# Performance work log

Hardware: AMD Instinct MI355X
Metric: run time of the kernel (lower is better)

The kernel has to match this reference:

```python
import math
import jax, jax.numpy as jnp
import numpy as np

B, S, D, QK, H = 4, 4096, 1024, 128, 2048  # hidden = int(2.0 * dim)
NUM_BUCKETS, MAX_DIST = 32, 128
LN_EPS = 1e-5


def setup_inputs() -> dict:
    key = jax.random.key(0)
    ks = jax.random.split(key, 7)
    x = jax.random.normal(ks[0], (B, S, D), jnp.float32)
    ln_g = jnp.ones((D,), jnp.float32)
    ln_b = jnp.zeros((D,), jnp.float32)
    Wh = jax.random.normal(ks[1], (D, 2 * H), jnp.float32) * 0.02
    bh = jnp.zeros((2 * H,), jnp.float32)
    Wqk = jax.random.normal(ks[2], (D, QK), jnp.float32) * 0.02
    bqk = jnp.zeros((QK,), jnp.float32)
    os_gamma = jax.random.normal(ks[3], (2, QK), jnp.float32) * 0.02  # nn.init.normal_(std=0.02)
    os_beta = jnp.zeros((2, QK), jnp.float32)
    Wo = jax.random.normal(ks[4], (H, D), jnp.float32) * 0.02
    bo = jnp.zeros((D,), jnp.float32)
    rel_emb = jax.random.normal(ks[5], (NUM_BUCKETS, 1), jnp.float32) * 0.02
    return {"x": x, "ln_g": ln_g, "ln_b": ln_b, "Wh": Wh, "bh": bh,
            "Wqk": Wqk, "bqk": bqk, "os_gamma": os_gamma, "os_beta": os_beta,
            "Wo": Wo, "bo": bo, "rel_emb": rel_emb}


def _t5_rel_bias(rel_emb, seq_len, scale):
    # non-causal T5 relative position bucket (num_buckets halved to 16)
    pos = jnp.arange(seq_len)
    rel = pos[None, :] - pos[:, None]  # k_pos - q_pos -> [i, j]
    n = -rel
    nb = NUM_BUCKETS // 2  # 16
    me = nb // 2           # max_exact = 8
    ret = (n < 0).astype(jnp.int32) * nb
    na = jnp.abs(n)
    val_large = me + (jnp.log(jnp.maximum(na, 1).astype(jnp.float32) / me)
                      / math.log(MAX_DIST / me) * (nb - me)).astype(jnp.int32)
    val_large = jnp.minimum(val_large, nb - 1)
    bucket = ret + jnp.where(na < me, na, val_large)  # [S, S] in [0, 31]
    return rel_emb[bucket, 0] * scale  # [S, S]


def reference(x, ln_g, ln_b, Wh, bh, Wqk, bqk, os_gamma, os_beta, Wo, bo, rel_emb):
    seq_len = x.shape[-2]
    # LayerNorm
    mu = jnp.mean(x, axis=-1, keepdims=True)
    var = jnp.mean(jnp.square(x - mu), axis=-1, keepdims=True)
    normed = (x - mu) * jax.lax.rsqrt(var + LN_EPS) * ln_g + ln_b
    # hidden (v, gate) with SiLU
    hidden = jax.nn.silu(normed @ Wh + bh)  # [B, S, 2H]
    v, gate = hidden[..., :H], hidden[..., H:]
    # qk projection + offset/scale into q, k
    qk = jax.nn.silu(normed @ Wqk + bqk)  # [B, S, QK]
    q = qk * os_gamma[0] + os_beta[0]
    k = qk * os_gamma[1] + os_beta[1]
    sim = jnp.einsum('bid,bjd->bij', q, k)  # [B, S, S]
    sim = sim + _t5_rel_bias(rel_emb, seq_len, float(D) ** 0.5)
    attn = jnp.square(jax.nn.relu(sim / seq_len))  # ReLU^2, no softmax
    out = jnp.einsum('bij,bjd->bid', attn, v) * gate  # [B, S, H]
    out = out @ Wo + bo
    return out + x  # add_residual
```

## Files before the change

### kernel.cpp

```cpp
#include <hip/hip_runtime.h>
#include <hip/hip_bf16.h>
#include <math.h>

typedef __bf16 bf16_t;
typedef __bf16 bf16x8 __attribute__((ext_vector_type(8)));
typedef __bf16 bf16x4 __attribute__((ext_vector_type(4)));
typedef float  f32x4  __attribute__((ext_vector_type(4)));

#define S_LEN 4096
#define D_DIM 1024
#define QK_DIM 128
#define H_DIM 2048
#define BATCH 4

__device__ __forceinline__ void gld_lds16(const void* g, void* l) {
  __builtin_amdgcn_global_load_lds((const __attribute__((address_space(1))) void*)g,
                                   (__attribute__((address_space(3))) void*)l, 16, 0, 0);
}

__device__ __forceinline__ float silu_f(float v) {
  return v / (1.0f + __expf(-v));
}

__device__ __forceinline__ float ldf(const void* p, size_t i, int f32) {
  return f32 ? ((const float*)p)[i] : (float)((const bf16_t*)p)[i];
}

__global__ void probe_k(const unsigned* __restrict__ ln_g_raw, int* __restrict__ flag) {
  if (threadIdx.x == 0) flag[0] = (ln_g_raw[0] == 0x3F800000u) ? 1 : 0;
}

#define M_HID 0
#define M_QK 1
#define M_SCORE 2
#define M_PV 3
#define M_OUT 4

template <int MODE>
__global__ __launch_bounds__(512)
void gemm256(const bf16_t* __restrict__ A, const bf16_t* __restrict__ Bt, int K,
             const void* e0, const void* e1, const float* __restrict__ ef,
             void* o0, void* o1, const int* __restrict__ dflag)
{
  constexpr int BMv = (MODE == M_PV) ? 128 : 256;
  constexpr int MR  = BMv / 32;
  constexpr int CA  = BMv / 128;
  constexpr int SA  = BMv * 64;
  constexpr int SB  = 256 * 64;

  __shared__ __align__(16) char lds[4 * SA + 4 * SB];
  char* ldsA = lds;
  char* ldsB = lds + 4 * SA;

  const int t = threadIdx.x;
  const int w = t >> 6, lane = t & 63;
  const int quad = lane >> 4, col = lane & 15;
  const int wm = (w >> 2) * (BMv / 2);
  const int wn = (w & 3) * 64;

  const int gx = gridDim.x;
  const int nwg = gx * (int)gridDim.y;
  const int orig = (int)blockIdx.y * gx + (int)blockIdx.x;
  const int wg = (orig & 7) * (nwg >> 3) + (orig >> 3);
  const int shx = __builtin_ctz(gx);
  const int bx = wg & (gx - 1), by = wg >> shx;
  const int m0 = bx * BMv, n0 = by * 256;

  size_t a_src[CA], b_src[2];
#pragma unroll
  for (int cc = 0; cc < CA; ++cc) {
    const int P = cc * 8192 + t * 16;
    const int L = P ^ (((P >> 7) & 3) << 4);
    a_src[cc] = (size_t)(m0 + (L >> 6)) * K + ((L & 63) >> 1);
  }
#pragma unroll
  for (int cc = 0; cc < 2; ++cc) {
    const int P = cc * 8192 + t * 16;
    const int L = P ^ (((P >> 7) & 3) << 4);
    b_src[cc] = (size_t)(n0 + (L >> 6)) * K + ((L & 63) >> 1);
  }

  const int xr = (((col >> 1) & 3) ^ quad) << 4;
  const int base_a = (wm + col) * 64 + xr;
  const int base_b = (wn + col) * 64 + xr;

  f32x4 acc[MR][4] = {};
  bf16x8 af[MR], bfr[4];

#define STAGE(pt) do {                                                         \
    char* la_ = ldsA + ((pt) & 3) * SA + w * 1024;                             \
    char* lb_ = ldsB + ((pt) & 3) * SB + w * 1024;                             \
    const bf16_t* ga_ = A + (size_t)(pt) * 32;                                 \
    const bf16_t* gb_ = Bt + (size_t)(pt) * 32;                                \
    _Pragma("unroll") for (int cc_ = 0; cc_ < CA; ++cc_)                       \
      gld_lds16(ga_ + a_src[cc_], la_ + cc_ * 8192);                           \
    gld_lds16(gb_ + b_src[0], lb_);                                            \
    gld_lds16(gb_ + b_src[1], lb_ + 8192);                                     \
  } while (0)

#define LOAD_FRAGS(p) do {                                                     \
    const char* as_ = ldsA + ((p) & 3) * SA;                                   \
    const char* bs_ = ldsB + ((p) & 3) * SB;                                   \
    _Pragma("unroll") for (int m_ = 0; m_ < MR; ++m_)                          \
      af[m_] = *(const bf16x8*)(as_ + base_a + m_ * 1024);                     \
    _Pragma("unroll") for (int n_ = 0; n_ < 4; ++n_)                           \
      bfr[n_] = *(const bf16x8*)(bs_ + base_b + n_ * 1024);                    \
  } while (0)

#define STEADY_WAIT() do {                                                     \
    if constexpr (CA == 2) asm volatile("s_waitcnt vmcnt(8)" ::: "memory");    \
    else                   asm volatile("s_waitcnt vmcnt(6)" ::: "memory");    \
  } while (0)
#define PEEL1_WAIT() do {                                                      \
    if constexpr (CA == 2) asm volatile("s_waitcnt vmcnt(4)" ::: "memory");    \
    else                   asm volatile("s_waitcnt vmcnt(3)" ::: "memory");    \
  } while (0)

#define BAR_MFMA() do {                                                        \
    __builtin_amdgcn_sched_barrier(0);                                         \
    __builtin_amdgcn_s_barrier();                                              \
    __builtin_amdgcn_sched_barrier(0);                                         \
    __builtin_amdgcn_s_setprio(1);                                             \
    _Pragma("unroll") for (int m_ = 0; m_ < MR; ++m_)                          \
      _Pragma("unroll") for (int n_ = 0; n_ < 4; ++n_)                         \
        acc[m_][n_] = __builtin_amdgcn_mfma_f32_16x16x32_bf16(                 \
            af[m_], bfr[n_], acc[m_][n_], 0, 0, 0);                            \
    __builtin_amdgcn_s_setprio(0);                                             \
    __builtin_amdgcn_sched_barrier(0);                                         \
    __builtin_amdgcn_s_barrier();                                              \
    __builtin_amdgcn_sched_barrier(0);                                         \
  } while (0)

  const int NT = K >> 5;

  STAGE(0); STAGE(1); STAGE(2);
  STEADY_WAIT();
  __builtin_amdgcn_s_barrier();

  for (int p = 0; p < NT - 3; ++p) {
    LOAD_FRAGS(p);
    STAGE(p + 3);
    STEADY_WAIT();
    BAR_MFMA();
  }
  LOAD_FRAGS(NT - 3);
  PEEL1_WAIT();
  BAR_MFMA();
  LOAD_FRAGS(NT - 2);
  asm volatile("s_waitcnt vmcnt(0)" ::: "memory");
  BAR_MFMA();
  LOAD_FRAGS(NT - 1);
  BAR_MFMA();

#undef STAGE
#undef LOAD_FRAGS
#undef STEADY_WAIT
#undef PEEL1_WAIT
#undef BAR_MFMA

  __syncthreads();

  int f32 = 0;
  if constexpr (MODE == M_HID || MODE == M_OUT) f32 = dflag[0];

  if constexpr (MODE == M_OUT) {
    float (*swzf)[16][68] = (float (*)[16][68])lds;
#pragma unroll
    for (int m = 0; m < MR; ++m) {
#pragma unroll
      for (int j = 0; j < 4; ++j)
#pragma unroll
        for (int r = 0; r < 4; ++r)
          swzf[w][quad * 4 + r][j * 16 + col] = acc[m][j][r];
#pragma unroll
      for (int it = 0; it < 4; ++it) {
        const int task = it * 64 + lane, gr = task >> 4, ch = task & 15;
        const int gm = m0 + wm + m * 16 + gr;
        const int gnc = n0 + wn + ch * 4;
        f32x4 vv = *(const f32x4*)&swzf[w][gr][ch * 4];
        float xr4[4], r4[4];
        if (f32) {
          float4 t4 = *(const float4*)((const float*)e1 + (size_t)gm * D_DIM + gnc);
          xr4[0] = t4.x; xr4[1] = t4.y; xr4[2] = t4.z; xr4[3] = t4.w;
        } else {
          bf16x4 t4 = *(const bf16x4*)((const bf16_t*)e1 + (size_t)gm * D_DIM + gnc);
#pragma unroll
          for (int qq = 0; qq < 4; ++qq) xr4[qq] = (float)t4[qq];
        }
#pragma unroll
        for (int qq = 0; qq < 4; ++qq)
          r4[qq] = vv[qq] + ldf(e0, gnc + qq, f32) + xr4[qq];
        if (f32) {
          float4 s4 = {r4[0], r4[1], r4[2], r4[3]};
          *(float4*)((float*)o0 + (size_t)gm * D_DIM + gnc) = s4;
        } else {
          bf16x4 s4;
#pragma unroll
          for (int qq = 0; qq < 4; ++qq) s4[qq] = (bf16_t)r4[qq];
          *(bf16x4*)((bf16_t*)o0 + (size_t)gm * D_DIM + gnc) = s4;
        }
      }
    }
    return;
  }

  if constexpr (MODE == M_HID) {
    if (n0 < H_DIM) {
      bf16_t (*swzT)[16][136] = (bf16_t (*)[16][136])lds;
      const int bb  = m0 >> 12;
      const int smb = (m0 + wm) & (S_LEN - 1);
#pragma unroll
      for (int j = 0; j < 4; ++j) {
        const int gnj = n0 + wn + j * 16;
        const float bhv = ldf(e0, gnj + col, f32);
#pragma unroll
        for (int m = 0; m < MR; ++m)
#pragma unroll
          for (int r = 0; r < 4; ++r)
            swzT[w][col][m * 16 + quad * 4 + r] = (bf16_t)silu_f(acc[m][j][r] + bhv);
#pragma unroll
        for (int it = 0; it < 4; ++it) {
          const int task = it * 64 + lane, gr = task >> 4, ch = task & 15;
          bf16x8 vv = *(const bf16x8*)&swzT[w][gr][ch * 8];
          const size_t off = ((size_t)bb * H_DIM + (gnj + gr)) * S_LEN + smb + ch * 8;
          *(bf16x8*)((bf16_t*)o0 + off) = vv;
        }
      }
      return;
    }
  }

  if constexpr (MODE == M_HID || MODE == M_SCORE || MODE == M_PV) {
    bf16_t (*swzb)[16][72] = (bf16_t (*)[16][72])lds;
#pragma unroll
    for (int m = 0; m < MR; ++m) {
#pragma unroll
      for (int j = 0; j < 4; ++j) {
        const int gn = n0 + wn + j * 16 + col;
#pragma unroll
        for (int r = 0; r < 4; ++r) {
          const float val = acc[m][j][r];
          bf16_t sv;
          if constexpr (MODE == M_HID) {
            sv = (bf16_t)silu_f(val + ldf(e0, gn, f32));
          } else if constexpr (MODE == M_SCORE) {
            const int gm = m0 + wm + m * 16 + quad * 4 + r;
            float wgt = fmaxf((val + ef[gm - gn + (S_LEN - 1)]) *
                              (1.0f / (float)S_LEN), 0.0f);
            sv = (bf16_t)(wgt * wgt);
          } else {
            sv = (bf16_t)val;
          }
          swzb[w][quad * 4 + r][j * 16 + col] = sv;
        }
      }
#pragma unroll
      for (int it = 0; it < 2; ++it) {
        const int task = it * 64 + lane, gr = task >> 3, ch = task & 7;
        const int gm  = m0 + wm + m * 16 + gr;
        const int gnb = n0 + wn + ch * 8;
        bf16x8 vv = *(const bf16x8*)&swzb[w][gr][ch * 8];
        if constexpr (MODE == M_HID) {
          *(bf16x8*)((bf16_t*)o1 + (size_t)gm * H_DIM + (gnb - H_DIM)) = vv;
        } else if constexpr (MODE == M_SCORE) {
          *(bf16x8*)((bf16_t*)o0 + (size_t)gm * S_LEN + gnb) = vv;
        } else {
          bf16x8 g8 = *(const bf16x8*)((const bf16_t*)e0 + (size_t)gm * H_DIM + gnb);
          bf16x8 r8;
#pragma unroll
          for (int qq = 0; qq < 8; ++qq)
            r8[qq] = (bf16_t)((float)vv[qq] * (float)g8[qq]);
          *(bf16x8*)((bf16_t*)o0 + (size_t)gm * H_DIM + gnb) = r8;
        }
      }
    }
  }
}

template <int MODE>
__global__ __launch_bounds__(256)
void gemm_bt(const bf16_t* __restrict__ A, const bf16_t* __restrict__ Bt,
             int M, int N, int K,
             const void* e0, const void* e1, const void* e2,
             const float* __restrict__ ef,
             void* o0, void* o1, const int* __restrict__ dflag)
{
  __shared__ __align__(16) bf16_t As[128 * 32];
  __shared__ __align__(16) bf16_t Bs[128 * 32];
  const int t = threadIdx.x;
  const int w = t >> 6, lane = t & 63;
  const int quad = lane >> 4, col = lane & 15;
  const int wm = (w >> 1) << 6, wn = (w & 1) << 6;
  const int m0 = blockIdx.x * 128, n0 = blockIdx.y * 128;
  const int f32 = dflag[0];

  f32x4 acc[4][4] = {};

  for (int k0 = 0; k0 < K; k0 += 32) {
    __syncthreads();
    for (int p = 0; p < 2; ++p) {
      const int chunk = w * 2 + p;
      const int fl = (chunk * 64 + lane) * 8;
      const int r = fl >> 5, c = fl & 31;
      gld_lds16(A  + (size_t)(m0 + r) * K + (k0 + c), &As[chunk * 512]);
      gld_lds16(Bt + (size_t)(n0 + r) * K + (k0 + c), &Bs[chunk * 512]);
    }
    __syncthreads();

    bf16x8 af[4], bfr[4];
#pragma unroll
    for (int i = 0; i < 4; ++i)
      af[i] = *(const bf16x8*)&As[(wm + i * 16 + col) * 32 + quad * 8];
#pragma unroll
    for (int i = 0; i < 4; ++i)
      bfr[i] = *(const bf16x8*)&Bs[(wn + i * 16 + col) * 32 + quad * 8];
#pragma unroll
    for (int i = 0; i < 4; ++i)
#pragma unroll
      for (int j = 0; j < 4; ++j)
        acc[i][j] = __builtin_amdgcn_mfma_f32_16x16x32_bf16(af[i], bfr[j], acc[i][j], 0, 0, 0);
  }

#pragma unroll
  for (int i = 0; i < 4; ++i) {
#pragma unroll
    for (int j = 0; j < 4; ++j) {
#pragma unroll
      for (int r = 0; r < 4; ++r) {
        const int gm = m0 + wm + i * 16 + quad * 4 + r;
        const int gn = n0 + wn + j * 16 + col;
        float val = acc[i][j][r] + ldf(e0, gn, f32);
        float s = silu_f(val);
        ((bf16_t*)o0)[(size_t)gm * QK_DIM + gn] =
            (bf16_t)(s * ldf(e1, gn, f32) + ldf(e2, gn, f32));
        ((bf16_t*)o1)[(size_t)gm * QK_DIM + gn] =
            (bf16_t)(s * ldf(e1, QK_DIM + gn, f32) + ldf(e2, QK_DIM + gn, f32));
      }
    }
  }
}

__global__ __launch_bounds__(256)
void layernorm_k(const void* __restrict__ x, const void* __restrict__ g,
                 const void* __restrict__ be, bf16_t* __restrict__ out,
                 const int* __restrict__ dflag)
{
  const int row = blockIdx.x;
  const int t = threadIdx.x;
  const int f32 = dflag[0];
  float f[4];
  if (f32) {
    const float* xr = (const float*)x + (size_t)row * D_DIM;
    float4 xv = *(const float4*)&xr[t * 4];
    f[0] = xv.x; f[1] = xv.y; f[2] = xv.z; f[3] = xv.w;
  } else {
    const bf16_t* xr = (const bf16_t*)x + (size_t)row * D_DIM;
    bf16x4 xv = *(const bf16x4*)&xr[t * 4];
#pragma unroll
    for (int i = 0; i < 4; ++i) f[i] = (float)xv[i];
  }
  float s = 0.f, sq = 0.f;
#pragma unroll
  for (int i = 0; i < 4; ++i) { s += f[i]; sq += f[i] * f[i]; }
#pragma unroll
  for (int off = 32; off > 0; off >>= 1) {
    s += __shfl_down(s, off);
    sq += __shfl_down(sq, off);
  }
  __shared__ float red[8];
  const int w = t >> 6;
  if ((t & 63) == 0) { red[w] = s; red[4 + w] = sq; }
  __syncthreads();
  s = red[0] + red[1] + red[2] + red[3];
  sq = red[4] + red[5] + red[6] + red[7];
  const float mu = s * (1.0f / D_DIM);
  const float var = sq * (1.0f / D_DIM) - mu * mu;
  const float inv = rsqrtf(var + 1e-5f);
  bf16x4 ov;
#pragma unroll
  for (int i = 0; i < 4; ++i) {
    float nv = (f[i] - mu) * inv * ldf(g, t * 4 + i, f32) + ldf(be, t * 4 + i, f32);
    ov[i] = (bf16_t)nv;
  }
  *(bf16x4*)&out[(size_t)row * D_DIM + t * 4] = ov;
}

__global__ __launch_bounds__(256)
void transpose_k(const void* __restrict__ src, bf16_t* __restrict__ dst,
                 int R, int C, const int* __restrict__ dflag)
{
  __shared__ bf16_t tile[32][33];
  const int f32 = dflag[0];
  const int c0 = blockIdx.x * 32, r0 = blockIdx.y * 32;
  for (int i = threadIdx.y; i < 32; i += 8)
    tile[i][threadIdx.x] = (bf16_t)ldf(src, (size_t)(r0 + i) * C + (c0 + threadIdx.x), f32);
  __syncthreads();
  for (int i = threadIdx.y; i < 32; i += 8)
    dst[(size_t)(c0 + i) * R + (r0 + threadIdx.x)] = tile[threadIdx.x][i];
}

__global__ void bias_k(const void* __restrict__ rel_emb, float* __restrict__ bias,
                       const int* __restrict__ dflag)
{
  int d = blockIdx.x * 256 + threadIdx.x;
  if (d >= 2 * S_LEN - 1) return;
  const int f32 = dflag[0];
  int n = d - (S_LEN - 1);
  int ret = (n < 0) ? 16 : 0;
  int na = n < 0 ? -n : n;
  int b;
  if (na < 8) b = na;
  else {
    float vl = logf((float)na * (1.0f / 8.0f)) / logf(16.0f) * 8.0f;
    int vi = 8 + (int)vl;
    b = vi > 15 ? 15 : vi;
  }
  bias[d] = ldf(rel_emb, ret + b, f32) * 32.0f;
}

extern "C" void kernel_launch(void* const* d_in, const int* in_sizes, int n_in,
                              void* d_out, int out_size, void* d_ws, size_t ws_size,
                              hipStream_t stream)
{
  const void* x    = d_in[0];
  const void* ln_g = d_in[1];
  const void* ln_b = d_in[2];
  const void* Wh   = d_in[3];
  const void* bh   = d_in[4];
  const void* Wqk  = d_in[5];
  const void* bqk  = d_in[6];
  const void* osg  = d_in[7];
  const void* osb  = d_in[8];
  const void* Wo   = d_in[9];
  const void* bo   = d_in[10];
  const void* rel  = d_in[11];

  const int BS = BATCH * S_LEN;
  char* p = (char*)d_ws;
  int*    flags  = (int*)p;     p += 256;
  float*  bias   = (float*)p;   p += (size_t)8192 * 4;
  bf16_t* WhT    = (bf16_t*)p;  p += (size_t)4096 * 1024 * 2;
  bf16_t* WqkT   = (bf16_t*)p;  p += (size_t)128 * 1024 * 2;
  bf16_t* WoT    = (bf16_t*)p;  p += (size_t)1024 * 2048 * 2;
  bf16_t* q      = (bf16_t*)p;  p += (size_t)BS * QK_DIM * 2;
  bf16_t* kk     = (bf16_t*)p;  p += (size_t)BS * QK_DIM * 2;
  bf16_t* vT     = (bf16_t*)p;  p += (size_t)BS * H_DIM * 2;
  bf16_t* gate   = (bf16_t*)p;  p += (size_t)BS * H_DIM * 2;
  bf16_t* normed = (bf16_t*)p;  p += (size_t)BS * D_DIM * 2;
  bf16_t* attn   = normed;
  bf16_t* pvg    = gate;

  probe_k<<<1, 64, 0, stream>>>((const unsigned*)ln_g, flags);
  bias_k<<<32, 256, 0, stream>>>(rel, bias, flags);
  transpose_k<<<dim3(4096 / 32, 1024 / 32), dim3(32, 8), 0, stream>>>(Wh, WhT, 1024, 4096, flags);
  transpose_k<<<dim3(128 / 32, 1024 / 32), dim3(32, 8), 0, stream>>>(Wqk, WqkT, 1024, 128, flags);
  transpose_k<<<dim3(1024 / 32, 2048 / 32), dim3(32, 8), 0, stream>>>(Wo, WoT, 2048, 1024, flags);
  layernorm_k<<<BS, 256, 0, stream>>>(x, ln_g, ln_b, normed, flags);

  gemm256<M_HID><<<dim3(BS / 256, 4096 / 256), 512, 0, stream>>>(
      normed, WhT, 1024, bh, nullptr, nullptr, vT, gate, flags);
  gemm_bt<M_QK><<<dim3(BS / 128, 1), 256, 0, stream>>>(
      normed, WqkT, BS, QK_DIM, 1024, bqk, osg, osb, nullptr, q, kk, flags);

  for (int b = 0; b < BATCH; ++b) {
    gemm256<M_SCORE><<<dim3(S_LEN / 256, S_LEN / 256), 512, 0, stream>>>(
        q + (size_t)b * S_LEN * QK_DIM, kk + (size_t)b * S_LEN * QK_DIM,
        QK_DIM, nullptr, nullptr, bias, attn, nullptr, flags);
    gemm256<M_PV><<<dim3(S_LEN / 128, H_DIM / 256), 512, 0, stream>>>(
        attn, vT + (size_t)b * S_LEN * H_DIM, S_LEN,
        gate + (size_t)b * S_LEN * H_DIM, nullptr, nullptr,
        pvg + (size_t)b * S_LEN * H_DIM, nullptr, flags);
  }

  gemm256<M_OUT><<<dim3(BS / 256, 1024 / 256), 512, 0, stream>>>(
      pvg, WoT, 2048, bo, x, nullptr, d_out, nullptr, flags);
}
```

Baseline: 839.3 us.

## Restructure GEMM main loop into 8-phase ping-pong schedule with K=64 tiles

Replaces the 4-stage K=32 pipelined GEMM main loop with a double-buffered K=64 tile. The MFMA work is split into four quadrant phases separated by barriers, and global-to-LDS loads for the next tiles are interleaved between them. A wider LDS swizzle is used for the 128-byte rows. The goal is to overlap LDS reads, global loads and MFMA work more finely and to halve the iteration count. In exchange there are more barriers per iteration, and the shallower prefetch (two buffers instead of four) may expose more memory latency.

```diff
diff --git a/kernel.cpp b/kernel.cpp
--- a/kernel.cpp
+++ b/kernel.cpp
@@ -38,19 +38,20 @@
 
 template <int MODE>
 __global__ __launch_bounds__(512)
-void gemm256(const bf16_t* __restrict__ A, const bf16_t* __restrict__ Bt, int K,
-             const void* e0, const void* e1, const float* __restrict__ ef,
-             void* o0, void* o1, const int* __restrict__ dflag)
+void gemm8p(const bf16_t* __restrict__ A, const bf16_t* __restrict__ Bt, int K,
+            const void* e0, const void* e1, const float* __restrict__ ef,
+            void* o0, void* o1, const int* __restrict__ dflag)
 {
   constexpr int BMv = (MODE == M_PV) ? 128 : 256;
   constexpr int MR  = BMv / 32;
-  constexpr int CA  = BMv / 128;
-  constexpr int SA  = BMv * 64;
-  constexpr int SB  = 256 * 64;
-
-  __shared__ __align__(16) char lds[4 * SA + 4 * SB];
-  char* ldsA = lds;
-  char* ldsB = lds + 4 * SA;
+  constexpr int MH  = MR / 2;
+  constexpr int AL  = BMv / 128;
+  constexpr int ATILE = BMv * 128;
+  constexpr int AHALF = ATILE / 2;
+
+  __shared__ __align__(16) char lds[2 * ATILE + 2 * 32768];
+  char* const ldsA = lds;
+  char* const ldsB = lds + 2 * ATILE;
 
   const int t = threadIdx.x;
   const int w = t >> 6, lane = t & 63;
@@ -62,101 +63,126 @@
   const int nwg = gx * (int)gridDim.y;
   const int orig = (int)blockIdx.y * gx + (int)blockIdx.x;
   const int wg = (orig & 7) * (nwg >> 3) + (orig >> 3);
-  const int shx = __builtin_ctz(gx);
-  const int bx = wg & (gx - 1), by = wg >> shx;
+  const int bx = wg & (gx - 1), by = wg >> __builtin_ctz(gx);
   const int m0 = bx * BMv, n0 = by * 256;
 
-  size_t a_src[CA], b_src[2];
-#pragma unroll
-  for (int cc = 0; cc < CA; ++cc) {
-    const int P = cc * 8192 + t * 16;
-    const int L = P ^ (((P >> 7) & 3) << 4);
-    a_src[cc] = (size_t)(m0 + (L >> 6)) * K + ((L & 63) >> 1);
-  }
-#pragma unroll
-  for (int cc = 0; cc < 2; ++cc) {
-    const int P = cc * 8192 + t * 16;
-    const int L = P ^ (((P >> 7) & 3) << 4);
-    b_src[cc] = (size_t)(n0 + (L >> 6)) * K + ((L & 63) >> 1);
-  }
-
-  const int xr = (((col >> 1) & 3) ^ quad) << 4;
-  const int base_a = (wm + col) * 64 + xr;
-  const int base_b = (wn + col) * 64 + xr;
+  const bf16_t* const Ap = A + (size_t)m0 * K;
+  const bf16_t* const Bp = Bt + (size_t)n0 * K;
+
+  int aoff[AL], boff[2];
+#pragma unroll
+  for (int c = 0; c < AL; ++c) {
+    const int P = c * 8192 + t * 16;
+    const int L = P ^ (((P >> 7) & 7) << 4);
+    aoff[c] = (L >> 7) * K + ((L & 127) >> 1);
+  }
+#pragma unroll
+  for (int c = 0; c < 2; ++c) {
+    const int P = c * 8192 + t * 16;
+    const int L = P ^ (((P >> 7) & 7) << 4);
+    boff[c] = (L >> 7) * K + ((L & 127) >> 1);
+  }
+
+  const int xrq = (quad ^ (col & 7)) << 4;
+  const int abase = (wm + col) * 128 + xrq;
+  const int bbase = (wn + col) * 128 + xrq;
 
   f32x4 acc[MR][4] = {};
-  bf16x8 af[MR], bfr[4];
-
-#define STAGE(pt) do {                                                         \
-    char* la_ = ldsA + ((pt) & 3) * SA + w * 1024;                             \
-    char* lb_ = ldsB + ((pt) & 3) * SB + w * 1024;                             \
-    const bf16_t* ga_ = A + (size_t)(pt) * 32;                                 \
-    const bf16_t* gb_ = Bt + (size_t)(pt) * 32;                                \
-    _Pragma("unroll") for (int cc_ = 0; cc_ < CA; ++cc_)                       \
-      gld_lds16(ga_ + a_src[cc_], la_ + cc_ * 8192);                           \
-    gld_lds16(gb_ + b_src[0], lb_);                                            \
-    gld_lds16(gb_ + b_src[1], lb_ + 8192);                                     \
+  bf16x8 aF[MH][2], b0[2][2], b1[2][2];
+
+#define SB() __builtin_amdgcn_sched_barrier(0)
+#define BAR() do { SB(); __builtin_amdgcn_s_barrier(); SB(); } while (0)
+
+#define RD_A(mhalf) do {                                                       \
+    const char* as_ = ldsA + buf * ATILE;                                      \
+    _Pragma("unroll") for (int mi = 0; mi < MH; ++mi)                          \
+    _Pragma("unroll") for (int s = 0; s < 2; ++s)                              \
+      aF[mi][s] = *(const bf16x8*)(as_ +                                       \
+          ((abase + ((mhalf) * MH + mi) * 2048) ^ (s << 6)));                  \
   } while (0)
 
-#define LOAD_FRAGS(p) do {                                                     \
-    const char* as_ = ldsA + ((p) & 3) * SA;                                   \
-    const char* bs_ = ldsB + ((p) & 3) * SB;                                   \
-    _Pragma("unroll") for (int m_ = 0; m_ < MR; ++m_)                          \
-      af[m_] = *(const bf16x8*)(as_ + base_a + m_ * 1024);                     \
-    _Pragma("unroll") for (int n_ = 0; n_ < 4; ++n_)                           \
-      bfr[n_] = *(const bf16x8*)(bs_ + base_b + n_ * 1024);                    \
+#define RD_B(dst, nhalf) do {                                                  \
+    const char* bs_ = ldsB + buf * 32768;                                      \
+    _Pragma("unroll") for (int ni = 0; ni < 2; ++ni)                           \
+    _Pragma("unroll") for (int s = 0; s < 2; ++s)                              \
+      dst[ni][s] = *(const bf16x8*)(bs_ +                                      \
+          ((bbase + ((nhalf) * 2 + ni) * 2048) ^ (s << 6)));                   \
   } while (0)
 
-#define STEADY_WAIT() do {                                                     \
-    if constexpr (CA == 2) asm volatile("s_waitcnt vmcnt(8)" ::: "memory");    \
-    else                   asm volatile("s_waitcnt vmcnt(6)" ::: "memory");    \
+#define MM(mhalf, nhalf, BF) do {                                              \
+    __builtin_amdgcn_s_setprio(1);                                             \
+    _Pragma("unroll") for (int mi = 0; mi < MH; ++mi)                          \
+    _Pragma("unroll") for (int ni = 0; ni < 2; ++ni)                           \
+    _Pragma("unroll") for (int s = 0; s < 2; ++s)                              \
+      acc[(mhalf) * MH + mi][(nhalf) * 2 + ni] =                               \
+        __builtin_amdgcn_mfma_f32_16x16x32_bf16(                               \
+            aF[mi][s], BF[ni][s], acc[(mhalf) * MH + mi][(nhalf) * 2 + ni],    \
+            0, 0, 0);                                                          \
+    __builtin_amdgcn_s_setprio(0);                                             \
   } while (0)
-#define PEEL1_WAIT() do {                                                      \
-    if constexpr (CA == 2) asm volatile("s_waitcnt vmcnt(4)" ::: "memory");    \
-    else                   asm volatile("s_waitcnt vmcnt(3)" ::: "memory");    \
+
+#define STG_A(tt) do {                                                         \
+    char* base_ = ldsA + ((tt) & 1) * ATILE + w * 1024;                        \
+    const bf16_t* g_ = Ap + (size_t)(tt) * 64;                                 \
+    _Pragma("unroll") for (int h_ = 0; h_ < 2; ++h_)                           \
+    _Pragma("unroll") for (int c_ = 0; c_ < AL; ++c_)                          \
+      gld_lds16(g_ + (size_t)(h_ * (BMv / 2)) * K + aoff[c_],                  \
+                base_ + h_ * AHALF + c_ * 8192);                               \
   } while (0)
 
-#define BAR_MFMA() do {                                                        \
-    __builtin_amdgcn_sched_barrier(0);                                         \
-    __builtin_amdgcn_s_barrier();                                              \
-    __builtin_amdgcn_sched_barrier(0);                                         \
-    __builtin_amdgcn_s_setprio(1);                                             \
-    _Pragma("unroll") for (int m_ = 0; m_ < MR; ++m_)                          \
-      _Pragma("unroll") for (int n_ = 0; n_ < 4; ++n_)                         \
-        acc[m_][n_] = __builtin_amdgcn_mfma_f32_16x16x32_bf16(                 \
-            af[m_], bfr[n_], acc[m_][n_], 0, 0, 0);                            \
-    __builtin_amdgcn_s_setprio(0);                                             \
-    __builtin_amdgcn_sched_barrier(0);                                         \
-    __builtin_amdgcn_s_barrier();                                              \
-    __builtin_amdgcn_sched_barrier(0);                                         \
+#define STG_B(tt, h) do {                                                      \
+    char* base_ = ldsB + ((tt) & 1) * 32768 + (h) * 16384 + w * 1024;          \
+    const bf16_t* g_ = Bp + (size_t)((h) * 128) * K + (size_t)(tt) * 64;       \
+    _Pragma("unroll") for (int c_ = 0; c_ < 2; ++c_)                           \
+      gld_lds16(g_ + boff[c_], base_ + c_ * 8192);                             \
   } while (0)
 
-  const int NT = K >> 5;
-
-  STAGE(0); STAGE(1); STAGE(2);
-  STEADY_WAIT();
-  __builtin_amdgcn_s_barrier();
-
-  for (int p = 0; p < NT - 3; ++p) {
-    LOAD_FRAGS(p);
-    STAGE(p + 3);
-    STEADY_WAIT();
-    BAR_MFMA();
-  }
-  LOAD_FRAGS(NT - 3);
-  PEEL1_WAIT();
-  BAR_MFMA();
-  LOAD_FRAGS(NT - 2);
-  asm volatile("s_waitcnt vmcnt(0)" ::: "memory");
-  BAR_MFMA();
-  LOAD_FRAGS(NT - 1);
-  BAR_MFMA();
-
-#undef STAGE
-#undef LOAD_FRAGS
-#undef STEADY_WAIT
-#undef PEEL1_WAIT
-#undef BAR_MFMA
+#define WAIT_STEADY() do {                                                     \
+    if constexpr (AL == 2) asm volatile("s_waitcnt vmcnt(4)" ::: "memory");    \
+    else                   asm volatile("s_waitcnt vmcnt(2)" ::: "memory");    \
+  } while (0)
+
+  const int NT = K >> 6;
+
+  STG_A(0); STG_B(0, 0); STG_B(0, 1); STG_A(1);
+  WAIT_STEADY();
+  BAR();
+
+  for (int tt = 0; tt < NT; ++tt) {
+    const int buf = tt & 1;
+    RD_A(0); RD_B(b0, 0);
+    if (tt + 1 < NT) STG_B(tt + 1, 0);
+    BAR();
+    MM(0, 0, b0);
+    BAR();
+    RD_B(b1, 1);
+    if (tt + 1 < NT) STG_B(tt + 1, 1);
+    BAR();
+    MM(0, 1, b1);
+    BAR();
+    RD_A(1);
+    BAR();
+    MM(1, 1, b1);
+    BAR();
+    if (tt + 2 < NT) STG_A(tt + 2);
+    BAR();
+    MM(1, 0, b0);
+    SB();
+    if (tt + 1 < NT) {
+      if (tt + 2 < NT) WAIT_STEADY();
+      else asm volatile("s_waitcnt vmcnt(0)" ::: "memory");
+    }
+    BAR();
+  }
+
+#undef SB
+#undef BAR
+#undef RD_A
+#undef RD_B
+#undef MM
+#undef STG_A
+#undef STG_B
+#undef WAIT_STEADY
 
   __syncthreads();
 
@@ -457,21 +483,21 @@
   transpose_k<<<dim3(1024 / 32, 2048 / 32), dim3(32, 8), 0, stream>>>(Wo, WoT, 2048, 1024, flags);
   layernorm_k<<<BS, 256, 0, stream>>>(x, ln_g, ln_b, normed, flags);
 
-  gemm256<M_HID><<<dim3(BS / 256, 4096 / 256), 512, 0, stream>>>(
+  gemm8p<M_HID><<<dim3(BS / 256, 4096 / 256), 512, 0, stream>>>(
       normed, WhT, 1024, bh, nullptr, nullptr, vT, gate, flags);
   gemm_bt<M_QK><<<dim3(BS / 128, 1), 256, 0, stream>>>(
       normed, WqkT, BS, QK_DIM, 1024, bqk, osg, osb, nullptr, q, kk, flags);
 
   for (int b = 0; b < BATCH; ++b) {
-    gemm256<M_SCORE><<<dim3(S_LEN / 256, S_LEN / 256), 512, 0, stream>>>(
+    gemm8p<M_SCORE><<<dim3(S_LEN / 256, S_LEN / 256), 512, 0, stream>>>(
         q + (size_t)b * S_LEN * QK_DIM, kk + (size_t)b * S_LEN * QK_DIM,
         QK_DIM, nullptr, nullptr, bias, attn, nullptr, flags);
-    gemm256<M_PV><<<dim3(S_LEN / 128, H_DIM / 256), 512, 0, stream>>>(
+    gemm8p<M_PV><<<dim3(S_LEN / 128, H_DIM / 256), 512, 0, stream>>>(
         attn, vT + (size_t)b * S_LEN * H_DIM, S_LEN,
         gate + (size_t)b * S_LEN * H_DIM, nullptr, nullptr,
         pvg + (size_t)b * S_LEN * H_DIM, nullptr, flags);
   }
 
-  gemm256<M_OUT><<<dim3(BS / 256, 1024 / 256), 512, 0, stream>>>(
+  gemm8p<M_OUT><<<dim3(BS / 256, 1024 / 256), 512, 0, stream>>>(
       pvg, WoT, 2048, bo, x, nullptr, d_out, nullptr, flags);
 }
```

After: 843.4 us. Within noise of the previous version (+0.5%).
